# Kernel tuning notes

Measured on AMD Instinct MI355X. Metric: run time of the kernel, lower is better.

Reference implementation:

```python
import jax, jax.numpy as jnp
import numpy as np

B, Cin, H, W = 8, 128, 64, 64
Cout, K, S, P = 128, 3, 1, 1
KK = K * K


def _conv(x, w, b=None):
    y = jax.lax.conv_general_dilated(
        x, w, window_strides=(S, S), padding=[(P, P), (P, P)],
        dimension_numbers=("NCHW", "OIHW", "NCHW"))
    if b is not None:
        y = y + b[None, :, None, None]
    return y


def setup_inputs() -> dict:
    key = jax.random.key(0)
    ks = jax.random.split(key, 6)
    x = jax.random.normal(ks[0], (B, Cin, H, W), jnp.float32)
    # offset/modulator convs are zero-init in the module; use small random
    # values so learned-offset sampling path is actually exercised.
    w_off = jax.random.normal(ks[1], (2 * KK, Cin, K, K), jnp.float32) * 0.01
    b_off = jax.random.normal(ks[2], (2 * KK,), jnp.float32) * 0.1
    w_mod = jax.random.normal(ks[3], (KK, Cin, K, K), jnp.float32) * 0.01
    b_mod = jax.random.normal(ks[4], (KK,), jnp.float32) * 0.1
    w_reg = jax.random.normal(ks[5], (Cout, Cin, K, K), jnp.float32) * (1.0 / np.sqrt(Cin * KK))
    return {"x": x, "w_off": w_off, "b_off": b_off,
            "w_mod": w_mod, "b_mod": b_mod, "w_reg": w_reg}


def _deform_conv2d(x, offset, mask, w_reg):
    # offset: [B, 2*KK, Hout, Wout] with (dy, dx) interleaved per tap (torchvision layout)
    Hout, Wout = offset.shape[2], offset.shape[3]
    off = offset.reshape(B, KK, 2, Hout, Wout)
    dy = off[:, :, 0].transpose(0, 2, 3, 1)  # [B,Hout,Wout,KK]
    dx = off[:, :, 1].transpose(0, 2, 3, 1)
    kh = (jnp.arange(KK) // K).astype(jnp.float32)
    kw = (jnp.arange(KK) % K).astype(jnp.float32)
    ho = jnp.arange(Hout, dtype=jnp.float32) * S - P
    wo = jnp.arange(Wout, dtype=jnp.float32) * S - P
    py = ho[None, :, None, None] + kh[None, None, None, :] + dy  # [B,Hout,Wout,KK]
    px = wo[None, None, :, None] + kw[None, None, None, :] + dx
    y0f = jnp.floor(py); x0f = jnp.floor(px)
    wy = (py - y0f)[..., None]; wx = (px - x0f)[..., None]
    y0 = y0f.astype(jnp.int32); x0 = x0f.astype(jnp.int32)
    x_bhwc = x.transpose(0, 2, 3, 1)  # [B,H,W,Cin]
    bidx = jnp.arange(B).reshape(B, 1, 1, 1)

    def gather(yi, xi):
        valid = ((yi >= 0) & (yi < H) & (xi >= 0) & (xi < W)).astype(x.dtype)
        v = x_bhwc[bidx, jnp.clip(yi, 0, H - 1), jnp.clip(xi, 0, W - 1)]
        return v * valid[..., None]  # [B,Hout,Wout,KK,Cin], zero outside

    v00 = gather(y0, x0)
    v01 = gather(y0, x0 + 1)
    v10 = gather(y0 + 1, x0)
    v11 = gather(y0 + 1, x0 + 1)
    val = (v00 * (1 - wy) * (1 - wx) + v01 * (1 - wy) * wx
           + v10 * wy * (1 - wx) + v11 * wy * wx)
    # modulated deformable conv v2: mask [B,KK,Hout,Wout]
    val = val * mask.transpose(0, 2, 3, 1)[..., None]
    # weighted accumulation over taps and input channels -> NCHW output
    return jnp.einsum("bhwkc,ock->bohw", val, w_reg.reshape(Cout, Cin, KK))


def reference(x, w_off, b_off, w_mod, b_mod, w_reg):
    offset = _conv(x, w_off, b_off)
    mask = 2.0 * jax.nn.sigmoid(_conv(x, w_mod, b_mod))
    return _deform_conv2d(x, offset, mask, w_reg)
```

## Files before the change

kernel.cpp:

```cpp
#include <hip/hip_runtime.h>
#include <hip/hip_bf16.h>
#include <math.h>

#define H 64
#define W 64
#define CIN 128
#define COUT 128
#define BATCH 8
#define NPIX (H*W)
#define PXT 32
#define AP  136
#define RP  36
#define VSZ (PXT*AP)

typedef __attribute__((ext_vector_type(8))) short bf16x8;
typedef __attribute__((ext_vector_type(4))) float f32x4;
typedef __attribute__((ext_vector_type(16))) float f32x16;

static __device__ inline short f2bf(float f) {
  union { float f; unsigned u; } v; v.f = f;
  unsigned r = v.u + 0x7FFF + ((v.u >> 16) & 1);
  return (short)(r >> 16);
}
static __device__ inline float bf_lo(unsigned u) {
  union { unsigned u; float f; } v; v.u = u << 16; return v.f;
}
static __device__ inline float bf_hi(unsigned u) {
  union { unsigned u; float f; } v; v.u = u & 0xffff0000u; return v.f;
}

__global__ __launch_bounds__(256) void k_prep(const float* __restrict__ x,
    short* __restrict__ xbh,
    const float* __restrict__ w_off, const float* __restrict__ w_mod,
    short* __restrict__ wOMs, const float* __restrict__ w_reg,
    short* __restrict__ wAs) {
  __shared__ float tile[32][65];
  int blk = blockIdx.x;
  int t = threadIdx.x;
  if (blk < 2048) {
    int cg = blk & 3, y = (blk >> 2) & 63, b = blk >> 8;
#pragma unroll
    for (int j = 0; j < 8; ++j) {
      int idx = t + j * 256;
      int ci = idx >> 6, xi = idx & 63;
      tile[ci][xi] = x[(((b * CIN + cg * 32 + ci) * H + y) * W) + xi];
    }
    __syncthreads();
#pragma unroll
    for (int j = 0; j < 8; ++j) {
      int idx = t + j * 256;
      int xi = idx >> 5, ci = idx & 31;
      xbh[((b * H + y) * W + xi) * CIN + cg * 32 + ci] = f2bf(tile[ci][xi]);
    }
  } else if (blk < 2048 + 144) {
    int e = (blk - 2048) * 256 + t;
    int tap = e >> 12, oc = (e >> 7) & 31, c = e & 127;
    float v = 0.f;
    if (oc < 18)      v = w_off[(oc * 128 + c) * 9 + tap];
    else if (oc < 27) v = w_mod[((oc - 18) * 128 + c) * 9 + tap];
    int kstep = c >> 4, g = (c >> 3) & 1, j = c & 7;
    int lane = g * 32 + oc;
    int o = ((tap * 8 + kstep) * 64 + lane) * 8 + j;
    wOMs[o] = f2bf(v);
  } else {
    int e = (blk - 2192) * 256 + t;
    int tap = e >> 14, oc = (e >> 7) & 127, c = e & 127;
    int kstep = c >> 4, g = (c >> 3) & 1, j = c & 7;
    int ms = oc >> 5, m = oc & 31;
    int lane = g * 32 + m;
    int o = (((tap * 8 + kstep) * 4 + ms) * 64 + lane) * 8 + j;
    wAs[o] = f2bf(w_reg[(oc * 128 + c) * 9 + tap]);
  }
}

__global__ __launch_bounds__(512, 8) void k_deform(const short* __restrict__ xbh,
    const short* __restrict__ wOMs, const float* __restrict__ b_off,
    const float* __restrict__ b_mod, const short* __restrict__ wAs,
    float* __restrict__ out) {
  __shared__ __align__(16) char smem_u[31104];
  __shared__ __align__(16) float  pw[PXT * 9 * 4];
  __shared__ __align__(16) ushort pa4[PXT * 9 * 4];
  float* red  = (float*)smem_u;
  short* vs   = (short*)smem_u;
  float* redE = (float*)smem_u;

  int blk = blockIdx.x;
  int b = blk & 7, tile = blk >> 3;
  int pix0 = tile * PXT;
  int t = threadIdx.x;
  int lane = t & 63;
  int wv = t >> 6;
  int n32 = lane & 31, g = lane >> 5;

  const short* xbB = xbh + (size_t)b * NPIX * CIN;

  {
    f32x16 accO = {};
#pragma unroll
    for (int ti = 0; ti < 2; ++ti) {
      int tap = wv + ti * 8;
      if (tap > 8) break;
      int dy = tap / 3 - 1, dx = tap % 3 - 1;
      int gp = pix0 + n32;
      int y = (gp >> 6) + dy, x = (gp & 63) + dx;
      int ok = ((unsigned)y < H) && ((unsigned)x < W);
      int lin = ok ? ((y << 6) + x) : 0;
      const short* wt = wOMs;
#pragma unroll
      for (int kstep = 0; kstep < 8; ++kstep) {
        bf16x8 a = *(const bf16x8*)&wt[((tap * 8 + kstep) * 64 + lane) * 8];
        int c0 = kstep * 16 + g * 8;
        bf16x8 bv = *(const bf16x8*)&xbB[(size_t)lin * CIN + c0];
        if (!ok) bv = (bf16x8){};
        accO = __builtin_amdgcn_mfma_f32_32x32x16_bf16(a, bv, accO, 0, 0, 0);
      }
    }
#pragma unroll
    for (int r = 0; r < 16; ++r) {
      int row = (r & 3) + 8 * (r >> 2) + 4 * g;
      if (row < 27) red[wv * (27 * RP) + row * RP + n32] = accO[r];
    }
  }
  __syncthreads();

  for (int i = t; i < PXT * 9; i += 512) {
    int tap = i % 9, p = i / 9;
    float dyv = b_off[2 * tap], dxv = b_off[2 * tap + 1], z = b_mod[tap];
#pragma unroll
    for (int w = 0; w < 8; ++w) {
      const float* rw = red + w * (27 * RP);
      dyv += rw[(2 * tap) * RP + p];
      dxv += rw[(2 * tap + 1) * RP + p];
      z   += rw[(18 + tap) * RP + p];
    }
    float m = 2.f / (1.f + expf(-z));
    int gp = pix0 + p;
    float py = (float)((gp >> 6) - 1 + tap / 3) + dyv;
    float pxx = (float)((gp & 63) - 1 + tap % 3) + dxv;
    float yf = floorf(py), xf = floorf(pxx);
    float wy = py - yf, wx = pxx - xf;
    int y0 = (int)yf, x0 = (int)xf;
    int y1 = y0 + 1, x1 = x0 + 1;
    float vy0 = ((unsigned)y0 < H) ? 1.f : 0.f;
    float vy1 = ((unsigned)y1 < H) ? 1.f : 0.f;
    float vx0 = ((unsigned)x0 < W) ? 1.f : 0.f;
    float vx1 = ((unsigned)x1 < W) ? 1.f : 0.f;
    int y0c = min(max(y0, 0), H - 1), y1c = min(max(y1, 0), H - 1);
    int x0c = min(max(x0, 0), W - 1), x1c = min(max(x1, 0), W - 1);
    *(float4*)&pw[i * 4] = make_float4((1.f - wy) * (1.f - wx) * m * vy0 * vx0,
                                       (1.f - wy) * wx * m * vy0 * vx1,
                                       wy * (1.f - wx) * m * vy1 * vx0,
                                       wy * wx * m * vy1 * vx1);
    pa4[i * 4 + 0] = (ushort)((y0c << 6) + x0c);
    pa4[i * 4 + 1] = (ushort)((y0c << 6) + x1c);
    pa4[i * 4 + 2] = (ushort)((y1c << 6) + x0c);
    pa4[i * 4 + 3] = (ushort)((y1c << 6) + x1c);
  }
  __syncthreads();

  int ms = wv & 3, ks = wv >> 2;
  int cq = t & 15, ps = t >> 4;
  int c0s = cq * 8;

  f32x16 acc = {};

  for (int tap = 0; tap < 9; ++tap) {
    short* vbuf = vs + (tap & 1) * VSZ;

    {
      int idx = (ps * 9 + tap) * 4;
      float4 wq = *(const float4*)&pw[idx];
      int a00 = (int)pa4[idx]     * CIN;
      int a01 = (int)pa4[idx + 1] * CIN;
      int a10 = (int)pa4[idx + 2] * CIN;
      int a11 = (int)pa4[idx + 3] * CIN;
      uint4 u00 = *(const uint4*)&xbB[a00 + c0s];
      uint4 u01 = *(const uint4*)&xbB[a01 + c0s];
      uint4 u10 = *(const uint4*)&xbB[a10 + c0s];
      uint4 u11 = *(const uint4*)&xbB[a11 + c0s];
      uint4 packed;
#pragma unroll
      for (int j = 0; j < 4; ++j) {
        unsigned ua = ((const unsigned*)&u00)[j];
        unsigned ub = ((const unsigned*)&u01)[j];
        unsigned uc = ((const unsigned*)&u10)[j];
        unsigned ud = ((const unsigned*)&u11)[j];
        float s0 = fmaf(wq.w, bf_lo(ud), fmaf(wq.z, bf_lo(uc),
                   fmaf(wq.y, bf_lo(ub), wq.x * bf_lo(ua))));
        float s1 = fmaf(wq.w, bf_hi(ud), fmaf(wq.z, bf_hi(uc),
                   fmaf(wq.y, bf_hi(ub), wq.x * bf_hi(ua))));
        __hip_bfloat162 h2 = __float22bfloat162_rn(make_float2(s0, s1));
        ((unsigned*)&packed)[j] = *(unsigned*)&h2;
      }
      *(uint4*)&vbuf[ps * AP + c0s] = packed;
    }

    bf16x8 af[4];
#pragma unroll
    for (int i = 0; i < 4; ++i) {
      int kstep = ks * 4 + i;
      af[i] = *(const bf16x8*)&wAs[(((tap * 8 + kstep) * 4 + ms) * 64 + lane) * 8];
    }
    __syncthreads();

#pragma unroll
    for (int i = 0; i < 4; ++i) {
      int kstep = ks * 4 + i;
      int c0 = kstep * 16 + g * 8;
      bf16x8 bfr = *(const bf16x8*)&vbuf[n32 * AP + c0];
      acc = __builtin_amdgcn_mfma_f32_32x32x16_bf16(af[i], bfr, acc, 0, 0, 0);
    }
  }

  __syncthreads();
  if (ks == 1) {
#pragma unroll
    for (int r = 0; r < 16; ++r) {
      int row = (r & 3) + 8 * (r >> 2) + 4 * g;
      redE[ms * (32 * 33) + row * 33 + n32] = acc[r];
    }
  }
  __syncthreads();
  if (ks == 0) {
#pragma unroll
    for (int r = 0; r < 16; ++r) {
      int row = (r & 3) + 8 * (r >> 2) + 4 * g;
      float v = acc[r] + redE[ms * (32 * 33) + row * 33 + n32];
      out[(size_t)(b * COUT + ms * 32 + row) * NPIX + pix0 + n32] = v;
    }
  }
}

extern "C" void kernel_launch(void* const* d_in, const int* in_sizes, int n_in,
                              void* d_out, int out_size, void* d_ws, size_t ws_size,
                              hipStream_t stream) {
  const float* x     = (const float*)d_in[0];
  const float* w_off = (const float*)d_in[1];
  const float* b_off = (const float*)d_in[2];
  const float* w_mod = (const float*)d_in[3];
  const float* b_mod = (const float*)d_in[4];
  const float* w_reg = (const float*)d_in[5];

  short* xbh  = (short*)d_ws;
  short* wAs  = xbh + 4194304;
  short* wOMs = wAs + 147456;
  float* out  = (float*)d_out;

  k_prep<<<dim3(2768), 256, 0, stream>>>(x, xbh, w_off, w_mod, wOMs,
                                         w_reg, wAs);
  k_deform<<<dim3(NPIX / PXT * BATCH), 512, 0, stream>>>(
      xbh, wOMs, b_off, b_mod, wAs, out);
}
```

Measured before the change: 112.1 us.

## Software-pipeline bilinear gather with MFMA across taps in deform kernel

Restructures the per-tap loop so the gathers and bilinear blend for tap+1 are issued before the MFMAs for the current tap, using the existing double buffer. A prologue fills the buffer for tap 0, and the weight fragments for the next tap are prefetched after the MFMAs. The goal is to hide global gather latency behind matrix math. In exchange, register pressure rises because the gathered vectors and the weight fragments stay live across the MFMAs, and this may hurt occupancy under launch_bounds(512,8).

After: 113.7 us. No clear change (+1.4%).

```diff
diff --git a/kernel.cpp b/kernel.cpp
--- a/kernel.cpp
+++ b/kernel.cpp
@@ -105,10 +105,9 @@
       int y = (gp >> 6) + dy, x = (gp & 63) + dx;
       int ok = ((unsigned)y < H) && ((unsigned)x < W);
       int lin = ok ? ((y << 6) + x) : 0;
-      const short* wt = wOMs;
 #pragma unroll
       for (int kstep = 0; kstep < 8; ++kstep) {
-        bf16x8 a = *(const bf16x8*)&wt[((tap * 8 + kstep) * 64 + lane) * 8];
+        bf16x8 a = *(const bf16x8*)&wOMs[((tap * 8 + kstep) * 64 + lane) * 8];
         int c0 = kstep * 16 + g * 8;
         bf16x8 bv = *(const bf16x8*)&xbB[(size_t)lin * CIN + c0];
         if (!ok) bv = (bf16x8){};
@@ -163,21 +162,61 @@
   int c0s = cq * 8;
 
   f32x16 acc = {};
+  bf16x8 af[4];
+
+  {
+    int idx = (ps * 9 + 0) * 4;
+    float4 wq = *(const float4*)&pw[idx];
+    uint4 u00 = *(const uint4*)&xbB[(int)pa4[idx]     * CIN + c0s];
+    uint4 u01 = *(const uint4*)&xbB[(int)pa4[idx + 1] * CIN + c0s];
+    uint4 u10 = *(const uint4*)&xbB[(int)pa4[idx + 2] * CIN + c0s];
+    uint4 u11 = *(const uint4*)&xbB[(int)pa4[idx + 3] * CIN + c0s];
+    uint4 packed;
+#pragma unroll
+    for (int j = 0; j < 4; ++j) {
+      unsigned ua = ((const unsigned*)&u00)[j];
+      unsigned ub = ((const unsigned*)&u01)[j];
+      unsigned uc = ((const unsigned*)&u10)[j];
+      unsigned ud = ((const unsigned*)&u11)[j];
+      float s0 = fmaf(wq.w, bf_lo(ud), fmaf(wq.z, bf_lo(uc),
+                 fmaf(wq.y, bf_lo(ub), wq.x * bf_lo(ua))));
+      float s1 = fmaf(wq.w, bf_hi(ud), fmaf(wq.z, bf_hi(uc),
+                 fmaf(wq.y, bf_hi(ub), wq.x * bf_hi(ua))));
+      __hip_bfloat162 h2 = __float22bfloat162_rn(make_float2(s0, s1));
+      ((unsigned*)&packed)[j] = *(unsigned*)&h2;
+    }
+    *(uint4*)&vs[ps * AP + c0s] = packed;
+#pragma unroll
+    for (int i = 0; i < 4; ++i) {
+      int kstep = ks * 4 + i;
+      af[i] = *(const bf16x8*)&wAs[(((0 * 8 + kstep) * 4 + ms) * 64 + lane) * 8];
+    }
+  }
+  __syncthreads();
 
   for (int tap = 0; tap < 9; ++tap) {
     short* vbuf = vs + (tap & 1) * VSZ;
-
-    {
-      int idx = (ps * 9 + tap) * 4;
-      float4 wq = *(const float4*)&pw[idx];
-      int a00 = (int)pa4[idx]     * CIN;
-      int a01 = (int)pa4[idx + 1] * CIN;
-      int a10 = (int)pa4[idx + 2] * CIN;
-      int a11 = (int)pa4[idx + 3] * CIN;
-      uint4 u00 = *(const uint4*)&xbB[a00 + c0s];
-      uint4 u01 = *(const uint4*)&xbB[a01 + c0s];
-      uint4 u10 = *(const uint4*)&xbB[a10 + c0s];
-      uint4 u11 = *(const uint4*)&xbB[a11 + c0s];
+    short* vnext = vs + ((tap + 1) & 1) * VSZ;
+
+    uint4 u00, u01, u10, u11; float4 wq;
+    if (tap < 8) {
+      int idx = (ps * 9 + tap + 1) * 4;
+      wq = *(const float4*)&pw[idx];
+      u00 = *(const uint4*)&xbB[(int)pa4[idx]     * CIN + c0s];
+      u01 = *(const uint4*)&xbB[(int)pa4[idx + 1] * CIN + c0s];
+      u10 = *(const uint4*)&xbB[(int)pa4[idx + 2] * CIN + c0s];
+      u11 = *(const uint4*)&xbB[(int)pa4[idx + 3] * CIN + c0s];
+    }
+
+#pragma unroll
+    for (int i = 0; i < 4; ++i) {
+      int kstep = ks * 4 + i;
+      int c0 = kstep * 16 + g * 8;
+      bf16x8 bfr = *(const bf16x8*)&vbuf[n32 * AP + c0];
+      acc = __builtin_amdgcn_mfma_f32_32x32x16_bf16(af[i], bfr, acc, 0, 0, 0);
+    }
+
+    if (tap < 8) {
       uint4 packed;
 #pragma unroll
       for (int j = 0; j < 4; ++j) {
@@ -192,23 +231,13 @@
         __hip_bfloat162 h2 = __float22bfloat162_rn(make_float2(s0, s1));
         ((unsigned*)&packed)[j] = *(unsigned*)&h2;
       }
-      *(uint4*)&vbuf[ps * AP + c0s] = packed;
-    }
-
-    bf16x8 af[4];
-#pragma unroll
-    for (int i = 0; i < 4; ++i) {
-      int kstep = ks * 4 + i;
-      af[i] = *(const bf16x8*)&wAs[(((tap * 8 + kstep) * 4 + ms) * 64 + lane) * 8];
-    }
-    __syncthreads();
-
-#pragma unroll
-    for (int i = 0; i < 4; ++i) {
-      int kstep = ks * 4 + i;
-      int c0 = kstep * 16 + g * 8;
-      bf16x8 bfr = *(const bf16x8*)&vbuf[n32 * AP + c0];
-      acc = __builtin_amdgcn_mfma_f32_32x32x16_bf16(af[i], bfr, acc, 0, 0, 0);
+      *(uint4*)&vnext[ps * AP + c0s] = packed;
+#pragma unroll
+      for (int i = 0; i < 4; ++i) {
+        int kstep = ks * 4 + i;
+        af[i] = *(const bf16x8*)&wAs[((((tap + 1) * 8 + kstep) * 4 + ms) * 64 + lane) * 8];
+      }
+      __syncthreads();
     }
   }
 
```

## Stage input halo in shared memory for offset conv and use atomic reduction

Applied to the files above, without the earlier changes.

The offset/mask convolution now loads a 3x34 pixel halo of the bf16 input into XOR-swizzled LDS once per block, and reads its B fragments from there instead of issuing repeated global loads per tap. The per-wave partial results are summed into a single LDS buffer with shared-memory atomicAdd, replacing the 8-way strided reduction buffer. The prep kernel's transpose store is also vectorized to write four bf16 values per store. The cost is an extra staging phase and barrier, and contended LDS float atomics.

After: 133.9 us. 19.4% more time.

```diff
diff --git a/kernel.cpp b/kernel.cpp
--- a/kernel.cpp
+++ b/kernel.cpp
@@ -10,7 +10,6 @@
 #define NPIX (H*W)
 #define PXT 32
 #define AP  136
-#define RP  36
 #define VSZ (PXT*AP)
 
 typedef __attribute__((ext_vector_type(8))) short bf16x8;
@@ -47,10 +46,18 @@
     }
     __syncthreads();
 #pragma unroll
-    for (int j = 0; j < 8; ++j) {
-      int idx = t + j * 256;
-      int xi = idx >> 5, ci = idx & 31;
-      xbh[((b * H + y) * W + xi) * CIN + cg * 32 + ci] = f2bf(tile[ci][xi]);
+    for (int i = 0; i < 2; ++i) {
+      int idx = t + i * 256;
+      int xi = idx >> 3, cig = idx & 7;
+      float f0 = tile[cig * 4 + 0][xi];
+      float f1 = tile[cig * 4 + 1][xi];
+      float f2 = tile[cig * 4 + 2][xi];
+      float f3 = tile[cig * 4 + 3][xi];
+      __hip_bfloat162 h01 = __float22bfloat162_rn(make_float2(f0, f1));
+      __hip_bfloat162 h23 = __float22bfloat162_rn(make_float2(f2, f3));
+      uint2 pk;
+      pk.x = *(unsigned*)&h01; pk.y = *(unsigned*)&h23;
+      *(uint2*)&xbh[((b * H + y) * W + xi) * CIN + cg * 32 + cig * 4] = pk;
     }
   } else if (blk < 2048 + 144) {
     int e = (blk - 2048) * 256 + t;
@@ -77,16 +84,18 @@
     const short* __restrict__ wOMs, const float* __restrict__ b_off,
     const float* __restrict__ b_mod, const short* __restrict__ wAs,
     float* __restrict__ out) {
-  __shared__ __align__(16) char smem_u[31104];
+  __shared__ __align__(16) char smem_u[29696];
   __shared__ __align__(16) float  pw[PXT * 9 * 4];
   __shared__ __align__(16) ushort pa4[PXT * 9 * 4];
-  float* red  = (float*)smem_u;
+  float* redA = (float*)smem_u;
+  short* halo = (short*)(smem_u + 3584);
   short* vs   = (short*)smem_u;
   float* redE = (float*)smem_u;
 
   int blk = blockIdx.x;
   int b = blk & 7, tile = blk >> 3;
   int pix0 = tile * PXT;
+  int y0r = pix0 >> 6, x0r = pix0 & 63;
   int t = threadIdx.x;
   int lane = t & 63;
   int wv = t >> 6;
@@ -94,6 +103,18 @@
 
   const short* xbB = xbh + (size_t)b * NPIX * CIN;
 
+  for (int i = t; i < 27 * 33; i += 512) redA[i] = 0.f;
+  for (int i = t; i < 3 * 34 * 16; i += 512) {
+    int row34 = i / 544, rem = i - row34 * 544;
+    int col = rem >> 4, ck = rem & 15;
+    int yy = y0r + row34 - 1, xx = x0r + col - 1;
+    bf16x8 v = {};
+    if ((unsigned)yy < H && (unsigned)xx < W)
+      v = *(const bf16x8*)&xbB[(size_t)((yy << 6) + xx) * CIN + ck * 8];
+    *(bf16x8*)&halo[((row34 * 34 + col) << 7) + ((ck ^ (col & 15)) << 3)] = v;
+  }
+  __syncthreads();
+
   {
     f32x16 accO = {};
 #pragma unroll
@@ -101,38 +122,30 @@
       int tap = wv + ti * 8;
       if (tap > 8) break;
       int dy = tap / 3 - 1, dx = tap % 3 - 1;
-      int gp = pix0 + n32;
-      int y = (gp >> 6) + dy, x = (gp & 63) + dx;
-      int ok = ((unsigned)y < H) && ((unsigned)x < W);
-      int lin = ok ? ((y << 6) + x) : 0;
-      const short* wt = wOMs;
+      int col = n32 + dx + 1;
+      int colbase = (((dy + 1) * 34 + col) << 7);
+      int sw = col & 15;
 #pragma unroll
       for (int kstep = 0; kstep < 8; ++kstep) {
-        bf16x8 a = *(const bf16x8*)&wt[((tap * 8 + kstep) * 64 + lane) * 8];
-        int c0 = kstep * 16 + g * 8;
-        bf16x8 bv = *(const bf16x8*)&xbB[(size_t)lin * CIN + c0];
-        if (!ok) bv = (bf16x8){};
+        bf16x8 a = *(const bf16x8*)&wOMs[((tap * 8 + kstep) * 64 + lane) * 8];
+        int ck = kstep * 2 + g;
+        bf16x8 bv = *(const bf16x8*)&halo[colbase + ((ck ^ sw) << 3)];
         accO = __builtin_amdgcn_mfma_f32_32x32x16_bf16(a, bv, accO, 0, 0, 0);
       }
     }
 #pragma unroll
     for (int r = 0; r < 16; ++r) {
       int row = (r & 3) + 8 * (r >> 2) + 4 * g;
-      if (row < 27) red[wv * (27 * RP) + row * RP + n32] = accO[r];
+      if (row < 27) atomicAdd(&redA[row * 33 + n32], accO[r]);
     }
   }
   __syncthreads();
 
   for (int i = t; i < PXT * 9; i += 512) {
     int tap = i % 9, p = i / 9;
-    float dyv = b_off[2 * tap], dxv = b_off[2 * tap + 1], z = b_mod[tap];
-#pragma unroll
-    for (int w = 0; w < 8; ++w) {
-      const float* rw = red + w * (27 * RP);
-      dyv += rw[(2 * tap) * RP + p];
-      dxv += rw[(2 * tap + 1) * RP + p];
-      z   += rw[(18 + tap) * RP + p];
-    }
+    float dyv = b_off[2 * tap]     + redA[(2 * tap) * 33 + p];
+    float dxv = b_off[2 * tap + 1] + redA[(2 * tap + 1) * 33 + p];
+    float z   = b_mod[tap]         + redA[(18 + tap) * 33 + p];
     float m = 2.f / (1.f + expf(-z));
     int gp = pix0 + p;
     float py = (float)((gp >> 6) - 1 + tap / 3) + dyv;
@@ -170,14 +183,10 @@
     {
       int idx = (ps * 9 + tap) * 4;
       float4 wq = *(const float4*)&pw[idx];
-      int a00 = (int)pa4[idx]     * CIN;
-      int a01 = (int)pa4[idx + 1] * CIN;
-      int a10 = (int)pa4[idx + 2] * CIN;
-      int a11 = (int)pa4[idx + 3] * CIN;
-      uint4 u00 = *(const uint4*)&xbB[a00 + c0s];
-      uint4 u01 = *(const uint4*)&xbB[a01 + c0s];
-      uint4 u10 = *(const uint4*)&xbB[a10 + c0s];
-      uint4 u11 = *(const uint4*)&xbB[a11 + c0s];
+      uint4 u00 = *(const uint4*)&xbB[(int)pa4[idx]     * CIN + c0s];
+      uint4 u01 = *(const uint4*)&xbB[(int)pa4[idx + 1] * CIN + c0s];
+      uint4 u10 = *(const uint4*)&xbB[(int)pa4[idx + 2] * CIN + c0s];
+      uint4 u11 = *(const uint4*)&xbB[(int)pa4[idx + 3] * CIN + c0s];
       uint4 packed;
 #pragma unroll
       for (int j = 0; j < 4; ++j) {
```
